# Performance work log

Measured on AMD Instinct MI355X. Metric: run time of the kernel, lower is better.

## Reference

```python
import jax, jax.numpy as jnp
import numpy as np
import math

E = 2048         # n_embd
H = 16           # num query head pairs (num_heads)
HKV = 8          # num_kv_heads
NREP = H // HKV  # 2
HD = E // H // 2 # head_dim = 64
DEPTH = 12
LAMBDA_INIT = 0.8 - 0.6 * math.exp(-0.3 * DEPTH)
EPS = 1e-6


def setup_inputs() -> dict:
    key = jax.random.key(0)
    ks = jax.random.split(key, 10)
    s = lambda fan_in: 1.0 / np.sqrt(fan_in)
    return {
        "x": jax.random.normal(ks[0], (2, 2048, E), jnp.float32),
        "Wq": jax.random.normal(ks[1], (E, E), jnp.float32) * s(E),
        "Wk": jax.random.normal(ks[2], (E, E // NREP), jnp.float32) * s(E),
        "Wv": jax.random.normal(ks[3], (E, E // NREP), jnp.float32) * s(E),
        "Wo": jax.random.normal(ks[4], (E, E), jnp.float32) * s(E),
        "lam_q1": jax.random.normal(ks[5], (HD,), jnp.float32) * 0.1,
        "lam_k1": jax.random.normal(ks[6], (HD,), jnp.float32) * 0.1,
        "lam_q2": jax.random.normal(ks[7], (HD,), jnp.float32) * 0.1,
        "lam_k2": jax.random.normal(ks[8], (HD,), jnp.float32) * 0.1,
        "g": jnp.ones((2 * HD,), jnp.float32),  # RMSNorm weight
    }


def _rotary(x, cos, sin):
    # x: [B, T, nh, HD]; cos/sin: [T, HD//2]
    d = x.shape[-1] // 2
    x1, x2 = x[..., :d], x[..., d:]
    c = cos[None, :, None, :]
    si = sin[None, :, None, :]
    return jnp.concatenate([x1 * c + x2 * si, -x1 * si + x2 * c], axis=-1)


def reference(x, Wq, Wk, Wv, Wo, lam_q1, lam_k1, lam_q2, lam_k2, g):
    B, T, _ = x.shape
    q = (x @ Wq).reshape(B, T, 2 * H, HD)
    k = (x @ Wk).reshape(B, T, 2 * HKV, HD)
    v = (x @ Wv).reshape(B, T, HKV, 2 * HD)

    inv_freq = 1.0 / (10000.0 ** (jnp.arange(0, HD, 2, dtype=jnp.float32) / HD))
    freqs = jnp.arange(T, dtype=jnp.float32)[:, None] * inv_freq[None, :]
    cos, sin = jnp.cos(freqs), jnp.sin(freqs)
    q = _rotary(q, cos, sin)
    k = _rotary(k, cos, sin)

    q = jnp.transpose(q, (0, 2, 1, 3)) * (HD ** -0.5)   # [B, 2H, T, HD]
    k = jnp.repeat(jnp.transpose(k, (0, 2, 1, 3)), NREP, axis=1)  # [B, 2H, T, HD]
    v = jnp.repeat(jnp.transpose(v, (0, 2, 1, 3)), NREP, axis=1)  # [B, H, T, 2HD]

    scores = jnp.einsum('bhtd,bhsd->bhts', q, k)
    scores = jnp.nan_to_num(scores)
    mask = jnp.triu(jnp.full((T, T), -jnp.inf, scores.dtype), 1)
    scores = scores + mask
    p = jax.nn.softmax(scores.astype(jnp.float32), axis=-1).astype(scores.dtype)

    lam1 = jnp.exp(jnp.sum(lam_q1 * lam_k1))
    lam2 = jnp.exp(jnp.sum(lam_q2 * lam_k2))
    lam = lam1 - lam2 + LAMBDA_INIT

    p = p.reshape(B, H, 2, T, T)
    diff = p[:, :, 0] - lam * p[:, :, 1]               # [B, H, T, T]
    attn = jnp.einsum('bhts,bhsd->bhtd', diff, v)      # [B, H, T, 2HD]

    # RMSNorm over last dim (2*HD)
    attn = attn * jax.lax.rsqrt(jnp.mean(attn * attn, axis=-1, keepdims=True) + EPS) * g
    attn = attn * (1.0 - LAMBDA_INIT)
    attn = jnp.transpose(attn, (0, 2, 1, 3)).reshape(B, T, E)
    return attn @ Wo
```

## Files before the change

### kernel.cpp

```cpp
#include <hip/hip_runtime.h>

#define T_SEQ 2048

typedef __bf16 bf16x8 __attribute__((ext_vector_type(8)));
typedef float f32x4 __attribute__((ext_vector_type(4)));
typedef unsigned short u16;

__device__ __forceinline__ u16 f2b(float f) {
  unsigned u = __float_as_uint(f);
  unsigned r = 0x7fffu + ((u >> 16) & 1u);
  return (u16)((u + r) >> 16);
}
__device__ __forceinline__ float b2f(u16 v) {
  return __uint_as_float(((unsigned)v) << 16);
}
__device__ __forceinline__ f32x4 mfma16(bf16x8 a, bf16x8 b, f32x4 c) {
  return __builtin_amdgcn_mfma_f32_16x16x32_bf16(a, b, c, 0, 0, 0);
}
__device__ __forceinline__ unsigned pkhi(float lo, float hi) {
  return __builtin_amdgcn_perm(__float_as_uint(hi), __float_as_uint(lo), 0x07060302u);
}
#if defined(__has_builtin)
#if __has_builtin(__builtin_amdgcn_exp2f)
#define HAVE_RAW_EXP2 1
#endif
#endif
__device__ __forceinline__ float exp2r(float x) {
#ifdef HAVE_RAW_EXP2
  return __builtin_amdgcn_exp2f(x);
#else
  float r;
  asm("v_exp_f32 %0, %1" : "=v"(r) : "v"(x));
  return r;
#endif
}
__device__ __forceinline__ void glds16(const void* g, void* s) {
  __builtin_amdgcn_global_load_lds(
      (const __attribute__((address_space(1))) void*)(uintptr_t)g,
      (__attribute__((address_space(3))) void*)(unsigned)(uintptr_t)s, 16, 0, 0);
}

__global__ void lam_kernel(const float* __restrict__ q1, const float* __restrict__ k1,
                           const float* __restrict__ q2, const float* __restrict__ k2,
                           float* __restrict__ outp) {
  int l = threadIdx.x;
  float a = q1[l] * k1[l];
  float c = q2[l] * k2[l];
  #pragma unroll
  for (int off = 32; off > 0; off >>= 1) {
    a += __shfl_down(a, off);
    c += __shfl_down(c, off);
  }
  if (l == 0) outp[0] = expf(a) - expf(c) + 0.7836057665316244f;
}

__global__ __launch_bounds__(256) void convert_kernel(const float* __restrict__ in,
                                                      u16* __restrict__ outp, int n) {
  int i = (blockIdx.x * 256 + threadIdx.x) * 4;
  if (i >= n) return;
  float4 v = *(const float4*)(in + i);
  ushort4 pk;
  pk.x = f2b(v.x); pk.y = f2b(v.y); pk.z = f2b(v.z); pk.w = f2b(v.w);
  *(ushort4*)(outp + i) = pk;
}

__global__ __launch_bounds__(256) void transposeW_kernel(const float* __restrict__ Wq,
                                                         const float* __restrict__ Wk,
                                                         const float* __restrict__ Wv,
                                                         const float* __restrict__ Wo,
                                                         u16* __restrict__ outp) {
  __shared__ float tile[32][33];
  const int ro0 = blockIdx.y * 32;
  const int r0 = blockIdx.x * 32;
  const float* src; int C, cbase;
  if (ro0 < 2048)      { src = Wq; C = 2048; cbase = 0; }
  else if (ro0 < 3072) { src = Wk; C = 1024; cbase = 2048; }
  else if (ro0 < 4096) { src = Wv; C = 1024; cbase = 3072; }
  else                 { src = Wo; C = 2048; cbase = 4096; }
  const int cs0 = ro0 - cbase;
  const int tx = threadIdx.x & 31, ty = threadIdx.x >> 5;
  #pragma unroll
  for (int k2 = 0; k2 < 4; k2++)
    tile[ty * 4 + k2][tx] = src[(size_t)(r0 + ty * 4 + k2) * C + cs0 + tx];
  __syncthreads();
  #pragma unroll
  for (int k2 = 0; k2 < 4; k2++)
    outp[(size_t)(ro0 + ty * 4 + k2) * 2048 + r0 + tx] = f2b(tile[tx][ty * 4 + k2]);
}

template <bool OUT_BF16>
__global__ __launch_bounds__(256) void gemm128_kernel(const u16* __restrict__ A,
                                                      const u16* __restrict__ BT,
                                                      void* __restrict__ C, int N, int K) {
  __shared__ alignas(16) u16 As[128 * 64];
  __shared__ alignas(16) u16 Bs[128 * 64];
  const int tid = threadIdx.x, w = tid >> 6, lane = tid & 63;
  const int l15 = lane & 15, quad = lane >> 4;
  const int m0 = blockIdx.y * 128, n0 = blockIdx.x * 128;
  const int wm = (w >> 1) * 64, wn = (w & 1) * 64;
  const int lr = lane >> 3, slot = lane & 7, csw = slot ^ lr;
  f32x4 acc[4][4];
  #pragma unroll
  for (int mt = 0; mt < 4; mt++)
    #pragma unroll
    for (int nt = 0; nt < 4; nt++) acc[mt][nt] = (f32x4){0.f, 0.f, 0.f, 0.f};
  const u16* Ag = A + (size_t)(m0 + w * 32 + lr) * K + csw * 8;
  const u16* Bg = BT + (size_t)(n0 + w * 32 + lr) * K + csw * 8;
  u16* Asd = As + (w * 32) * 64;
  u16* Bsd = Bs + (w * 32) * 64;
  for (int kt = 0; kt < K; kt += 64) {
    #pragma unroll
    for (int i = 0; i < 4; i++) {
      glds16(Ag + kt + (size_t)(i * 8) * K, Asd + i * 512);
      glds16(Bg + kt + (size_t)(i * 8) * K, Bsd + i * 512);
    }
    __syncthreads();
    #pragma unroll
    for (int kk = 0; kk < 2; kk++) {
      bf16x8 am[4], bn[4];
      #pragma unroll
      for (int t = 0; t < 4; t++) {
        const int ra = wm + t * 16 + l15;
        am[t] = *(const bf16x8*)&As[ra * 64 + (((kk * 4 + quad) ^ (ra & 7)) << 3)];
        const int rb = wn + t * 16 + l15;
        bn[t] = *(const bf16x8*)&Bs[rb * 64 + (((kk * 4 + quad) ^ (rb & 7)) << 3)];
      }
      #pragma unroll
      for (int mt = 0; mt < 4; mt++)
        #pragma unroll
        for (int nt = 0; nt < 4; nt++) acc[mt][nt] = mfma16(am[mt], bn[nt], acc[mt][nt]);
    }
    __syncthreads();
  }
  const int row = m0 + wm + quad * 4;
  #pragma unroll
  for (int mt = 0; mt < 4; mt++) {
    #pragma unroll
    for (int nt = 0; nt < 4; nt++) {
      const int col = n0 + wn + nt * 16 + l15;
      #pragma unroll
      for (int rr = 0; rr < 4; rr++) {
        if (OUT_BF16)
          ((u16*)C)[(size_t)(row + mt * 16 + rr) * N + col] = f2b(acc[mt][nt][rr]);
        else
          ((float*)C)[(size_t)(row + mt * 16 + rr) * N + col] = acc[mt][nt][rr];
      }
    }
  }
}

#define STAGE_HALF(TILE, ROLE, BUF)                                                     \
  do {                                                                                  \
    const u16* sp_ = ((ROLE) == 0 || (ROLE) == 3 ? Ag : Bg) +                           \
                     (size_t)((ROLE) >= 2 ? 128 : 0) * K + (size_t)(TILE) * 64;         \
    u16* dp_ = ((ROLE) == 0 || (ROLE) == 3 ? &As[BUF][0] : &Bs[BUF][0]) +               \
               (((ROLE) >= 2 ? 128 : 0) + w * 8) * 64;                                  \
    glds16(sp_, dp_);                                                                   \
    glds16(sp_ + (size_t)64 * K, dp_ + 4096);                                           \
  } while (0)

#define PHASE(I, J, BUF, NEWA, NEWB, BN, STILE, SROLE, SBUF, DOVM)                      \
  do {                                                                                  \
    if (NEWA) {                                                                         \
      _Pragma("unroll") for (int u_ = 0; u_ < 4; u_++) {                                \
        const int ar_ = ((I) * 4 + u_) * 32 + wm * 16 + l15;                            \
        _Pragma("unroll") for (int kk_ = 0; kk_ < 2; kk_++)                             \
            am[u_][kk_] = *(const bf16x8*)&As[BUF][ar_ * 64 +                           \
                              (((kk_ * 4 + quad) ^ (ar_ & 7)) << 3)];                   \
      }                                                                                 \
    }                                                                                   \
    if (NEWB) {                                                                         \
      _Pragma("unroll") for (int v_ = 0; v_ < 2; v_++) {                                \
        const int br_ = ((J) * 2 + v_) * 64 + wn * 16 + l15;                            \
        _Pragma("unroll") for (int kk_ = 0; kk_ < 2; kk_++)                             \
            BN[v_][kk_] = *(const bf16x8*)&Bs[BUF][br_ * 64 +                           \
                              (((kk_ * 4 + quad) ^ (br_ & 7)) << 3)];                   \
      }                                                                                 \
    }                                                                                   \
    STAGE_HALF(STILE, SROLE, SBUF);                                                     \
    __builtin_amdgcn_s_barrier();                                                       \
    asm volatile("s_waitcnt lgkmcnt(0)" ::: "memory");                                  \
    __builtin_amdgcn_sched_barrier(0);                                                  \
    __builtin_amdgcn_s_setprio(1);                                                      \
    _Pragma("unroll") for (int u_ = 0; u_ < 4; u_++)                                    \
        _Pragma("unroll") for (int v_ = 0; v_ < 2; v_++) {                              \
      acc[(I) * 4 + u_][(J) * 2 + v_] =                                                 \
          mfma16(am[u_][0], BN[v_][0], acc[(I) * 4 + u_][(J) * 2 + v_]);                \
      acc[(I) * 4 + u_][(J) * 2 + v_] =                                                 \
          mfma16(am[u_][1], BN[v_][1], acc[(I) * 4 + u_][(J) * 2 + v_]);                \
    }                                                                                   \
    __builtin_amdgcn_s_setprio(0);                                                      \
    if (DOVM) asm volatile("s_waitcnt vmcnt(6)" ::: "memory");                          \
    __builtin_amdgcn_s_barrier();                                                       \
  } while (0)

__global__ __launch_bounds__(512, 2) void gemm256_kernel(const u16* __restrict__ A,
                                                         const u16* __restrict__ BT,
                                                         u16* __restrict__ C, int N, int K) {
  __shared__ alignas(16) u16 As[2][256 * 64];
  __shared__ alignas(16) u16 Bs[2][256 * 64];
  const int tid = threadIdx.x, w = tid >> 6, lane = tid & 63;
  const int l15 = lane & 15, quad = lane >> 4;
  const int wm = w >> 2, wn = w & 3;
  const int lr = lane >> 3, slot = lane & 7, csw = slot ^ lr;
  const int m0 = blockIdx.y * 256, n0 = blockIdx.x * 256;
  const int nkt = K >> 6;

  f32x4 acc[8][4];
  #pragma unroll
  for (int r = 0; r < 8; r++)
    #pragma unroll
    for (int s = 0; s < 4; s++) acc[r][s] = (f32x4){0.f, 0.f, 0.f, 0.f};

  const u16* Ag = A + (size_t)(m0 + w * 8 + lr) * K + csw * 8;
  const u16* Bg = BT + (size_t)(n0 + w * 8 + lr) * K + csw * 8;

  bf16x8 am[4][2], bn0[2][2], bn1[2][2];

  STAGE_HALF(0, 0, 0); STAGE_HALF(0, 1, 0); STAGE_HALF(0, 2, 0); STAGE_HALF(0, 3, 0);
  STAGE_HALF(1, 0, 1); STAGE_HALF(1, 1, 1); STAGE_HALF(1, 2, 1);
  asm volatile("s_waitcnt vmcnt(6)" ::: "memory");
  __builtin_amdgcn_s_barrier();

  #pragma unroll 1
  for (int t = 0; t < nkt; t += 2) {
    PHASE(0, 0, 0, 1, 1, bn0, t + 1, 3, 1, 0);
    PHASE(0, 1, 0, 0, 1, bn1, t + 2, 0, 0, 0);
    PHASE(1, 0, 0, 1, 0, bn0, t + 2, 1, 0, 0);
    PHASE(1, 1, 0, 0, 0, bn1, t + 2, 2, 0, 1);
    PHASE(0, 0, 1, 1, 1, bn0, t + 2, 3, 0, 0);
    PHASE(0, 1, 1, 0, 1, bn1, t + 3, 0, 1, 0);
    PHASE(1, 0, 1, 1, 0, bn0, t + 3, 1, 1, 0);
    PHASE(1, 1, 1, 0, 0, bn1, t + 3, 2, 1, 1);
  }

  const int crow = m0 + wm * 16 + quad * 4;
  const int ccol = n0 + wn * 16 + l15;
  #pragma unroll
  for (int r = 0; r < 8; r++)
    #pragma unroll
    for (int s = 0; s < 4; s++)
      #pragma unroll
      for (int rr = 0; rr < 4; rr++)
        C[(size_t)(crow + r * 32 + rr) * N + ccol + s * 64] = f2b(acc[r][s][rr]);
}

__global__ __launch_bounds__(256) void rotary_kernel(const u16* __restrict__ qkv,
                                                     u16* __restrict__ Qb,
                                                     u16* __restrict__ Kb, float qscale) {
  int idx = blockIdx.x * 256 + threadIdx.x;
  int i = idx & 31;
  int bt = (idx >> 5) & 4095;
  int hh = idx >> 17;
  int t = bt & (T_SEQ - 1), b = bt >> 11;
  bool isq = hh < 32;
  int col = isq ? hh * 64 : 2048 + (hh - 32) * 64;
  size_t inb = (size_t)bt * 4096 + col + i;
  float x1 = b2f(qkv[inb]);
  float x2 = b2f(qkv[inb + 32]);
  float invf = exp2f(-(float)i * 0.4152410118609203f);
  float ang = (float)t * invf;
  float c = cosf(ang), s = sinf(ang);
  float scale = isq ? qscale : 1.0f;
  float o1 = (x1 * c + x2 * s) * scale;
  float o2 = (x2 * c - x1 * s) * scale;
  u16* outp = isq ? (Qb + (size_t)(b * 32 + hh) * (T_SEQ * 64))
                  : (Kb + (size_t)(b * 16 + hh - 32) * (T_SEQ * 64));
  size_t ob = (size_t)t * 64 + i;
  outp[ob] = f2b(o1);
  outp[ob + 32] = f2b(o2);
}

__global__ __launch_bounds__(256) void vtrans_kernel(const u16* __restrict__ qkv,
                                                     u16* __restrict__ outp) {
  __shared__ unsigned tile[32][33];
  int bh = blockIdx.z;
  int t0 = blockIdx.x * 32, dv0 = blockIdx.y * 32;
  int tx = threadIdx.x & 31, ty = threadIdx.x >> 5;
  int bt_base = (bh >> 3) * T_SEQ;
  int col = 3072 + (bh & 7) * 128 + dv0 + tx;
  #pragma unroll
  for (int k2 = 0; k2 < 4; k2++)
    tile[ty * 4 + k2][tx] = qkv[(size_t)(bt_base + t0 + ty * 4 + k2) * 4096 + col];
  __syncthreads();
  const int stile = t0 >> 6, sin = (t0 & 63) + tx;
  #pragma unroll
  for (int k2 = 0; k2 < 4; k2++) {
    int dv = dv0 + ty * 4 + k2;
    outp[(((size_t)bh * 32 + stile) * 128 + dv) * 64 + sin] = (u16)tile[tx][ty * 4 + k2];
  }
}

__global__ __launch_bounds__(256) void attn_kernel(const u16* __restrict__ Qb,
                                                   const u16* __restrict__ Kb,
                                                   const u16* __restrict__ Vt,
                                                   const float* __restrict__ lamp,
                                                   const float* __restrict__ g,
                                                   u16* __restrict__ attn_out) {
  __shared__ alignas(16) u16 Ks[64 * 64];
  __shared__ alignas(16) u16 Vs[128 * 64];
  __shared__ alignas(16) u16 Ps[4][16][136];
  const int pr = blockIdx.x;
  const int bh = blockIdx.y;
  const int b = bh >> 4, h = bh & 15;
  const int tid = threadIdx.x, w = tid >> 6, lane = tid & 63;
  const int l15 = lane & 15, quad = lane >> 4;
  const int lr = lane >> 3, slot = lane & 7, csw = slot ^ lr;
  const float lam = lamp[0];

  const u16* Kg = Kb + (size_t)(b * 16 + h) * (T_SEQ * 64) + (w * 16 + lr) * 64 + csw * 8;
  const u16* Vg = Vt + (size_t)(b * 8 + (h >> 1)) * (T_SEQ * 128) + w * 2048 + lr * 64 + csw * 8;
  u16* kd = &Ks[w * 1024];
  u16* vd = &Vs[w * 2048];

  #pragma unroll 1
  for (int half = 0; half < 2; half++) {
    const int tt = half ? 31 - pr : pr;
    const int qb = tt * 64 + w * 16;
    const int qglob = qb + l15;

    bf16x8 qf[2][2];
    #pragma unroll
    for (int e = 0; e < 2; e++)
      #pragma unroll
      for (int kk = 0; kk < 2; kk++)
        qf[e][kk] = *(const bf16x8*)&Qb[((size_t)(b * 32 + 2 * h + e) * T_SEQ + qb + l15) * 64 +
                                        kk * 32 + quad * 8];

    f32x4 o[2][8];
    float lsum[2] = {0.f, 0.f};
    #pragma unroll
    for (int e = 0; e < 2; e++)
      #pragma unroll
      for (int nt = 0; nt < 8; nt++) o[e][nt] = (f32x4){0.f, 0.f, 0.f, 0.f};

    for (int st = 0; st <= tt; st++) {
      const u16* kp = Kg + st * 4096;
      const u16* vp = Vg + st * 8192;
      glds16(kp, kd); glds16(kp + 512, kd + 512);
      glds16(vp, vd); glds16(vp + 512, vd + 512);
      glds16(vp + 1024, vd + 1024); glds16(vp + 1536, vd + 1536);
      __syncthreads();

      bf16x8 kf[4][2];
      #pragma unroll
      for (int j = 0; j < 4; j++) {
        const int rk = j * 16 + l15;
        #pragma unroll
        for (int kk = 0; kk < 2; kk++)
          kf[j][kk] = *(const bf16x8*)&Ks[rk * 64 + (((kk * 4 + quad) ^ (rk & 7)) << 3)];
      }

      #pragma unroll
      for (int e = 0; e < 2; e++) {
        f32x4 sc[4];
        #pragma unroll
        for (int j = 0; j < 4; j++) {
          f32x4 z = {0.f, 0.f, 0.f, 0.f};
          z = mfma16(kf[j][0], qf[e][0], z);
          sc[j] = mfma16(kf[j][1], qf[e][1], z);
        }
        if (st == tt) {
          #pragma unroll
          for (int j = 0; j < 4; j++) {
            int srow = st * 64 + j * 16 + quad * 4;
            #pragma unroll
            for (int rr = 0; rr < 4; rr++)
              if (srow + rr > qglob) sc[j][rr] = -1e30f;
          }
        }
        float ls = 0.f;
        #pragma unroll
        for (int j = 0; j < 4; j++) {
          #pragma unroll
          for (int rr = 0; rr < 4; rr++) {
            float p = exp2r(sc[j][rr]);
            sc[j][rr] = p;
            ls += p;
          }
          uint2 pk;
          pk.x = pkhi(sc[j][0], sc[j][1]);
          pk.y = pkhi(sc[j][2], sc[j][3]);
          *(uint2*)&Ps[w][l15][e * 64 + j * 16 + quad * 4] = pk;
        }
        lsum[e] += ls;
      }
      asm volatile("s_waitcnt lgkmcnt(0)" ::: "memory");
      bf16x8 pa[2][2];
      #pragma unroll
      for (int e = 0; e < 2; e++)
        #pragma unroll
        for (int kk = 0; kk < 2; kk++)
          pa[e][kk] = *(const bf16x8*)&Ps[w][l15][e * 64 + kk * 32 + quad * 8];
      asm volatile("" ::: "memory");
      #pragma unroll
      for (int nt = 0; nt < 8; nt++) {
        const int rv = nt * 16 + l15;
        bf16x8 vf0 = *(const bf16x8*)&Vs[rv * 64 + ((quad ^ (rv & 7)) << 3)];
        bf16x8 vf1 = *(const bf16x8*)&Vs[rv * 64 + (((4 + quad) ^ (rv & 7)) << 3)];
        o[0][nt] = mfma16(vf0, pa[0][0], o[0][nt]);
        o[0][nt] = mfma16(vf1, pa[0][1], o[0][nt]);
        o[1][nt] = mfma16(vf0, pa[1][0], o[1][nt]);
        o[1][nt] = mfma16(vf1, pa[1][1], o[1][nt]);
      }
      __syncthreads();
    }

    float l0 = lsum[0], l1 = lsum[1];
    l0 += __shfl_xor(l0, 16); l0 += __shfl_xor(l0, 32);
    l1 += __shfl_xor(l1, 16); l1 += __shfl_xor(l1, 32);
    const float il0 = 1.f / l0, il1 = lam / l1;
    float ssq = 0.f;
    #pragma unroll
    for (int nt = 0; nt < 8; nt++)
      #pragma unroll
      for (int rr = 0; rr < 4; rr++) {
        float v = o[0][nt][rr] * il0 - o[1][nt][rr] * il1;
        o[0][nt][rr] = v;
        ssq += v * v;
      }
    ssq += __shfl_xor(ssq, 16);
    ssq += __shfl_xor(ssq, 32);
    const float rsc = rsqrtf(ssq * (1.f / 128.f) + 1e-6f) * 0.2163942334683756f;
    #pragma unroll
    for (int nt = 0; nt < 8; nt++) {
      float4 gv = *(const float4*)&g[nt * 16 + quad * 4];
      uint2 pk;
      pk.x = (unsigned)f2b(o[0][nt][0] * rsc * gv.x) |
             ((unsigned)f2b(o[0][nt][1] * rsc * gv.y) << 16);
      pk.y = (unsigned)f2b(o[0][nt][2] * rsc * gv.z) |
             ((unsigned)f2b(o[0][nt][3] * rsc * gv.w) << 16);
      *(uint2*)&Ps[w][l15][nt * 16 + quad * 4] = pk;
    }
    asm volatile("s_waitcnt lgkmcnt(0)" ::: "memory");
    #pragma unroll
    for (int i = 0; i < 4; i++) {
      const int r = (lane >> 4) + i * 4, c = (lane & 15) * 8;
      bf16x8 ov = *(const bf16x8*)&Ps[w][r][c];
      *(bf16x8*)&attn_out[(size_t)(b * T_SEQ + qb + r) * 2048 + h * 128 + c] = ov;
    }
    __syncthreads();
  }
}

extern "C" void kernel_launch(void* const* d_in, const int* in_sizes, int n_in, void* d_out,
                              int out_size, void* d_ws, size_t ws_size, hipStream_t stream) {
  const float* x = (const float*)d_in[0];
  const float* Wq = (const float*)d_in[1];
  const float* Wk = (const float*)d_in[2];
  const float* Wv = (const float*)d_in[3];
  const float* Wo = (const float*)d_in[4];
  const float* lq1 = (const float*)d_in[5];
  const float* lk1 = (const float*)d_in[6];
  const float* lq2 = (const float*)d_in[7];
  const float* lk2 = (const float*)d_in[8];
  const float* g = (const float*)d_in[9];

  char* ws = (char*)d_ws;
  u16* WT = (u16*)(ws);
  u16* xbf = (u16*)(ws + 25165824);
  u16* QKV = (u16*)(ws + 41943040);
  u16* Qb = (u16*)(ws + 75497472);
  u16* Kb = (u16*)(ws + 92274688);
  u16* Vt = (u16*)(ws + 100663296);
  u16* Attn = (u16*)(ws + 109051904);
  float* lam = (float*)(ws + 125829120);

  lam_kernel<<<1, 64, 0, stream>>>(lq1, lk1, lq2, lk2, lam);
  convert_kernel<<<8192, 256, 0, stream>>>(x, xbf, 8388608);
  transposeW_kernel<<<dim3(64, 192), 256, 0, stream>>>(Wq, Wk, Wv, Wo, WT);
  gemm256_kernel<<<dim3(16, 16), 512, 0, stream>>>(xbf, WT, QKV, 4096, 2048);
  rotary_kernel<<<24576, 256, 0, stream>>>(QKV, Qb, Kb, 0.18033688011112042f);
  vtrans_kernel<<<dim3(64, 4, 16), 256, 0, stream>>>(QKV, Vt);
  attn_kernel<<<dim3(16, 32), 256, 0, stream>>>(Qb, Kb, Vt, lam, g, Attn);
  gemm128_kernel<false><<<dim3(16, 32), 256, 0, stream>>>(Attn, WT + (size_t)4096 * 2048, d_out,
                                                          2048, 2048);
}
```

Measured before the change: 337.8 us.

## Double-buffer K/V tiles in attention loop and raise MFMA wave priority

Turns the single K/V shared-memory buffer into a double buffer, so the global-to-LDS copy for the next key tile is issued before computing on the current tile. This hides load latency and drops one barrier per iteration. It also raises wave priority around the MFMA blocks and pads the P scratch rows from 136 to 152. In exchange, LDS use roughly doubles, which may lower occupancy, and correctness depends on the async copy completing before the barrier at the end of each iteration.

```diff
diff --git a/kernel.cpp b/kernel.cpp
--- a/kernel.cpp
+++ b/kernel.cpp
@@ -297,9 +297,9 @@
                                                    const float* __restrict__ lamp,
                                                    const float* __restrict__ g,
                                                    u16* __restrict__ attn_out) {
-  __shared__ alignas(16) u16 Ks[64 * 64];
-  __shared__ alignas(16) u16 Vs[128 * 64];
-  __shared__ alignas(16) u16 Ps[4][16][136];
+  __shared__ alignas(16) u16 Ks[2][64 * 64];
+  __shared__ alignas(16) u16 Vs[2][128 * 64];
+  __shared__ alignas(16) u16 Ps[4][16][152];
   const int pr = blockIdx.x;
   const int bh = blockIdx.y;
   const int b = bh >> 4, h = bh & 15;
@@ -310,8 +310,8 @@
 
   const u16* Kg = Kb + (size_t)(b * 16 + h) * (T_SEQ * 64) + (w * 16 + lr) * 64 + csw * 8;
   const u16* Vg = Vt + (size_t)(b * 8 + (h >> 1)) * (T_SEQ * 128) + w * 2048 + lr * 64 + csw * 8;
-  u16* kd = &Ks[w * 1024];
-  u16* vd = &Vs[w * 2048];
+  u16* kd[2] = {&Ks[0][w * 1024], &Ks[1][w * 1024]};
+  u16* vd[2] = {&Vs[0][w * 2048], &Vs[1][w * 2048]};
 
   #pragma unroll 1
   for (int half = 0; half < 2; half++) {
@@ -334,13 +334,23 @@
       #pragma unroll
       for (int nt = 0; nt < 8; nt++) o[e][nt] = (f32x4){0.f, 0.f, 0.f, 0.f};
 
+    {
+      glds16(Kg, kd[0]); glds16(Kg + 512, kd[0] + 512);
+      glds16(Vg, vd[0]); glds16(Vg + 512, vd[0] + 512);
+      glds16(Vg + 1024, vd[0] + 1024); glds16(Vg + 1536, vd[0] + 1536);
+    }
+    __syncthreads();
+
+    #pragma unroll 1
     for (int st = 0; st <= tt; st++) {
-      const u16* kp = Kg + st * 4096;
-      const u16* vp = Vg + st * 8192;
-      glds16(kp, kd); glds16(kp + 512, kd + 512);
-      glds16(vp, vd); glds16(vp + 512, vd + 512);
-      glds16(vp + 1024, vd + 1024); glds16(vp + 1536, vd + 1536);
-      __syncthreads();
+      const int buf = st & 1;
+      if (st < tt) {
+        const u16* kp = Kg + (size_t)(st + 1) * 4096;
+        const u16* vp = Vg + (size_t)(st + 1) * 8192;
+        glds16(kp, kd[buf ^ 1]); glds16(kp + 512, kd[buf ^ 1] + 512);
+        glds16(vp, vd[buf ^ 1]); glds16(vp + 512, vd[buf ^ 1] + 512);
+        glds16(vp + 1024, vd[buf ^ 1] + 1024); glds16(vp + 1536, vd[buf ^ 1] + 1536);
+      }
 
       bf16x8 kf[4][2];
       #pragma unroll
@@ -348,18 +358,20 @@
         const int rk = j * 16 + l15;
         #pragma unroll
         for (int kk = 0; kk < 2; kk++)
-          kf[j][kk] = *(const bf16x8*)&Ks[rk * 64 + (((kk * 4 + quad) ^ (rk & 7)) << 3)];
+          kf[j][kk] = *(const bf16x8*)&Ks[buf][rk * 64 + (((kk * 4 + quad) ^ (rk & 7)) << 3)];
       }
 
       #pragma unroll
       for (int e = 0; e < 2; e++) {
         f32x4 sc[4];
+        __builtin_amdgcn_s_setprio(1);
         #pragma unroll
         for (int j = 0; j < 4; j++) {
           f32x4 z = {0.f, 0.f, 0.f, 0.f};
           z = mfma16(kf[j][0], qf[e][0], z);
           sc[j] = mfma16(kf[j][1], qf[e][1], z);
         }
+        __builtin_amdgcn_s_setprio(0);
         if (st == tt) {
           #pragma unroll
           for (int j = 0; j < 4; j++) {
@@ -393,16 +405,18 @@
         for (int kk = 0; kk < 2; kk++)
           pa[e][kk] = *(const bf16x8*)&Ps[w][l15][e * 64 + kk * 32 + quad * 8];
       asm volatile("" ::: "memory");
+      __builtin_amdgcn_s_setprio(1);
       #pragma unroll
       for (int nt = 0; nt < 8; nt++) {
         const int rv = nt * 16 + l15;
-        bf16x8 vf0 = *(const bf16x8*)&Vs[rv * 64 + ((quad ^ (rv & 7)) << 3)];
-        bf16x8 vf1 = *(const bf16x8*)&Vs[rv * 64 + (((4 + quad) ^ (rv & 7)) << 3)];
+        bf16x8 vf0 = *(const bf16x8*)&Vs[buf][rv * 64 + ((quad ^ (rv & 7)) << 3)];
+        bf16x8 vf1 = *(const bf16x8*)&Vs[buf][rv * 64 + (((4 + quad) ^ (rv & 7)) << 3)];
         o[0][nt] = mfma16(vf0, pa[0][0], o[0][nt]);
         o[0][nt] = mfma16(vf1, pa[0][1], o[0][nt]);
         o[1][nt] = mfma16(vf0, pa[1][0], o[1][nt]);
         o[1][nt] = mfma16(vf1, pa[1][1], o[1][nt]);
       }
+      __builtin_amdgcn_s_setprio(0);
       __syncthreads();
     }
 
```

Result: no change. 341.8 us (+1.2%).
